# Kernel tuning notes

Hardware: AMD Instinct MI355X
Metric: run time of the kernel (lower is better)

## Reference

```python
import jax, jax.numpy as jnp
import numpy as np

TAU = 0.1  # args.aggregator_tau


def _l2_normalize(x, eps=1e-12):
    # F.normalize(x) : dim=1, p=2, eps clamp on the norm
    n = jnp.linalg.norm(x, axis=1, keepdims=True)
    return x / jnp.maximum(n, eps)


def setup_inputs() -> dict:
    key = jax.random.key(0)
    ks = jax.random.split(key, 9)
    N_LB, N_ULB, D, C = 4096, 6144, 128, 100
    return {
        "anchor_feat": jax.random.normal(ks[0], (N_ULB, D), dtype=jnp.float32),
        "positive_feat": jax.random.normal(ks[1], (N_ULB, D), dtype=jnp.float32),
        "lb_feat": jax.random.normal(ks[2], (N_LB, D), dtype=jnp.float32),
        "lb_one_hot": jax.random.uniform(ks[3], (N_LB, C), dtype=jnp.float32),
        "logits_x_lb": jax.random.normal(ks[4], (N_LB, C), dtype=jnp.float32),
        "logits_x_ulb_1": jax.random.normal(ks[5], (N_ULB, C), dtype=jnp.float32),
        "logits_x_ulb_2": jax.random.normal(ks[6], (N_ULB, C), dtype=jnp.float32),
        "labels_lb": jax.random.randint(ks[7], (N_LB,), 0, C, dtype=jnp.int64),
        "labels_ulb": jax.random.randint(ks[8], (N_ULB,), 0, C, dtype=jnp.int64),
    }


def reference(anchor_feat, positive_feat, lb_feat, lb_one_hot,
              logits_x_lb, logits_x_ulb_1, logits_x_ulb_2,
              labels_lb, labels_ulb):
    normed_lb = _l2_normalize(lb_feat)
    anchor_q = _l2_normalize(anchor_feat)
    positive_q = _l2_normalize(positive_feat)
    # [N, D] with N = N_lb + 2*N_ulb
    feats = jnp.concatenate([normed_lb, anchor_q, positive_q], axis=0)
    logits_before = jnp.concatenate([logits_x_lb, logits_x_ulb_1, logits_x_ulb_2], axis=0)  # [N, C]

    # topk(k=1) over classes
    pred_before = jnp.argmax(logits_before, axis=1)            # [N]
    max_before = jnp.max(logits_before, axis=1)                # [N]

    # non-parametric self-attention aggregation: softmax(FF^T/tau) @ logits
    sim = (feats @ feats.T) / TAU                              # [N, N] large intermediate
    attn = jax.nn.softmax(sim, axis=1)
    logits_after = attn @ logits_before                        # [N, C]

    pred_after = jnp.argmax(logits_after, axis=1)
    max_after = jnp.max(logits_after, axis=1)

    changed = pred_before != pred_after                        # [N] bool
    # Original applies Softmax(dim=1) to [M,1,1] slices of the k=1 top logits,
    # which is identically 1.0, so diff_agg is all zeros; replicate literally.
    diff = jnp.abs(jax.nn.softmax(max_before[:, None], axis=1)
                   - jax.nn.softmax(max_after[:, None], axis=1))[:, 0]  # [N], zeros

    # argmax/argmin restricted to changed indices (first changed idx under ties,
    # matching torch argmax over changed_pred_idx-ordered zeros)
    max_diff_idx = jnp.argmax(jnp.where(changed, diff, -jnp.inf))
    min_diff_idx = jnp.argmin(jnp.where(changed, diff, jnp.inf))

    pred_max_diff_bf = pred_before[max_diff_idx]
    pred_max_diff_af = pred_after[max_diff_idx]
    pred_min_diff_bf = pred_before[min_diff_idx]
    pred_min_diff_af = pred_after[min_diff_idx]

    num_lb = logits_x_lb.shape[0]
    out_lb = logits_after[:num_lb]
    out_ulb = logits_after[num_lb:]
    n_ulb = out_ulb.shape[0] // 2
    out_ulb_1, out_ulb_2 = out_ulb[:n_ulb], out_ulb[n_ulb:]

    return (anchor_feat, positive_feat, lb_feat, lb_one_hot,
            out_lb, out_ulb_1, out_ulb_2,
            max_diff_idx, min_diff_idx,
            pred_max_diff_bf, pred_max_diff_af,
            pred_min_diff_bf, pred_min_diff_af)
```

## Files before the change

### kernel.cpp

```cpp
#include <hip/hip_runtime.h>
#include <hip/hip_bf16.h>

typedef unsigned short u16;
typedef unsigned int u32;
typedef __attribute__((ext_vector_type(8))) short short8;
typedef __attribute__((ext_vector_type(4))) float f32x4;

#define N_LB   4096
#define N_ULB  6144
#define N_TOT  16384
#define D      128
#define C      100
#define CT     104
#define PSTR   104

#define OFF_ANCHOR 0
#define OFF_POS    786432
#define OFF_LBF    1572864
#define OFF_OH     2097152
#define OFF_OUTLB  2506752
#define OFF_SCAL   4145152

__device__ __forceinline__ void split_bf16(float x, u16& hi, u16& lo) {
    __hip_bfloat16 h = __float2bfloat16(x);
    float r = x - __bfloat162float(h);
    __hip_bfloat16 l = __float2bfloat16(r);
    hi = __bfloat16_as_ushort(h);
    lo = __bfloat16_as_ushort(l);
}

__device__ __forceinline__ void gl_lds16(const char* g, char* l) {
    __builtin_amdgcn_global_load_lds(
        (const __attribute__((address_space(1))) u32*)g,
        (__attribute__((address_space(3))) u32*)l, 16, 0, 0);
}

__global__ void prep_all(const float* __restrict__ anchor,
                         const float* __restrict__ positive,
                         const float* __restrict__ lbf,
                         const float* __restrict__ l_lb,
                         const float* __restrict__ l_u1,
                         const float* __restrict__ l_u2,
                         u16* __restrict__ F2, u16* __restrict__ LT,
                         int* __restrict__ predB,
                         float* __restrict__ out)
{
    const int r = blockIdx.x;
    const int t = threadIdx.x;
    const float* fsrc; const float* lsrc; int rr, ptbase;
    if (r < N_LB)              { fsrc = lbf;      lsrc = l_lb; rr = r;                ptbase = OFF_LBF; }
    else if (r < N_LB + N_ULB) { fsrc = anchor;   lsrc = l_u1; rr = r - N_LB;         ptbase = OFF_ANCHOR; }
    else                       { fsrc = positive; lsrc = l_u2; rr = r - N_LB - N_ULB; ptbase = OFF_POS; }

    float2 x = *(const float2*)&fsrc[rr * D + 2 * t];
    float ss = x.x * x.x + x.y * x.y;
    #pragma unroll
    for (int m = 32; m; m >>= 1) ss += __shfl_xor(ss, m);
    float inv = 1.0f / fmaxf(sqrtf(ss), 1e-12f);
    u16 h0, l0, h1, l1;
    split_bf16(x.x * inv, h0, l0);
    split_bf16(x.y * inv, h1, l1);
    *(u32*)&F2[r * 256 + 2 * t]       = (u32)h0 | ((u32)h1 << 16);
    *(u32*)&F2[r * 256 + 128 + 2 * t] = (u32)l0 | ((u32)l1 << 16);
    *(float2*)&out[ptbase + rr * D + 2 * t] = x;

    const int pc = (r & ~31) | (((r >> 2) & 3) << 3) | ((r & 3) << 1) | ((r >> 4) & 1);
    float v0 = lsrc[rr * C + t];
    const int c1 = t + 64;
    float v1 = (c1 < C) ? lsrc[rr * C + c1] : 0.0f;
    u16 h, l;
    split_bf16(v0, h, l);
    LT[(size_t)(0 * CT + t) * N_TOT + pc] = h;
    LT[(size_t)(1 * CT + t) * N_TOT + pc] = l;
    if (c1 < CT) {
        float v = (c1 < C) ? v1 : ((c1 == C) ? 1.0f : 0.0f);
        split_bf16(v, h, l);
        LT[(size_t)(0 * CT + c1) * N_TOT + pc] = h;
        LT[(size_t)(1 * CT + c1) * N_TOT + pc] = l;
    }
    float bv = v0; int bi = t;
    if (c1 < C && v1 > bv) { bv = v1; bi = c1; }
    #pragma unroll
    for (int m = 32; m; m >>= 1) {
        float ov = __shfl_xor(bv, m);
        int   oi = __shfl_xor(bi, m);
        if (ov > bv || (ov == bv && oi < bi)) { bv = ov; bi = oi; }
    }
    if (t == 0) predB[r] = bi;
}

__global__ void copy_oh(const float4* __restrict__ oh, float4* __restrict__ out)
{
    for (int i = blockIdx.x * blockDim.x + threadIdx.x; i < N_LB * C / 4;
         i += gridDim.x * blockDim.x)
        out[i] = oh[i];
}

#define SK_BYTES  (64 * 512)
#define SLT_BYTES (112 * 256)

__launch_bounds__(512, 1)
__global__ void attn_mfma(const u16* __restrict__ F2, const u16* __restrict__ LT,
                          float* __restrict__ parts)
{
    __shared__ __align__(16) char smem[2 * SK_BYTES + 2 * SLT_BYTES];
    char* const sK0  = smem;
    char* const sK1  = smem + SK_BYTES;
    char* const sLT0 = smem + 2 * SK_BYTES;
    char* const sLT1 = smem + 2 * SK_BYTES + SLT_BYTES;

    const int tid  = threadIdx.x;
    const int lane = tid & 63;
    const int w    = tid >> 6;
    const int mq   = w >> 1;
    const int nqh  = w & 1;
    const int g    = lane >> 4;
    const int lr   = lane & 15;
    const int kh   = blockIdx.x & 1;
    const int qb   = blockIdx.x >> 1;
    const int q0   = qb * 128;
    const int KB0  = kh * 8192;

    const char* F2b = (const char*)F2;
    const char* LTb = (const char*)LT;

    if (tid < 256) {
        char* dst = (tid >> 7) ? sLT1 : sLT0;
        int row = 104 + ((tid & 127) >> 4), gr = tid & 15;
        *(f32x4*)(dst + row * 256 + gr * 16) = f32x4{0, 0, 0, 0};
    }

    short8 qhi[2][4], qlo[2][4];
    #pragma unroll
    for (int ms = 0; ms < 2; ++ms) {
        const char* base = F2b + (size_t)(q0 + mq * 32 + ms * 16 + lr) * 512;
        #pragma unroll
        for (int ks = 0; ks < 4; ++ks) {
            qhi[ms][ks] = *(const short8*)(base + ks * 64 + g * 16);
            qlo[ms][ks] = *(const short8*)(base + 256 + ks * 64 + g * 16);
        }
    }

    #pragma unroll
    for (int it = 0; it < 4; ++it) {
        int idx = tid + it * 512;
        int row = idx >> 5, b = (idx & 31) << 4;
        gl_lds16(F2b + (size_t)(KB0 + row) * 512 + (b ^ ((row & 15) << 4)),
                 sK0 + idx * 16);
    }
    #pragma unroll
    for (int it = 0; it < 4; ++it) {
        int idx = tid + it * 512;
        if (idx < 1664) {
            int row = idx >> 4, b = (idx & 15) << 4;
            int b2 = b ^ ((row & 7) << 4);
            int pl = b2 >> 7, kb2 = b2 & 127;
            gl_lds16(LTb + ((size_t)(pl * CT + row) * N_TOT + KB0) * 2 + kb2,
                     sLT0 + idx * 16);
        }
    }

    f32x4 o[2][7];
    #pragma unroll
    for (int ms = 0; ms < 2; ++ms)
        #pragma unroll
        for (int ct = 0; ct < 7; ++ct) o[ms][ct] = f32x4{0, 0, 0, 0};

    for (int ch = 0; ch < 128; ++ch) {
        const int cur = ch & 1;
        __syncthreads();

        if (ch + 1 < 128) {
            const int cn = KB0 + (ch + 1) * 64;
            char* dK = cur ? sK0 : sK1;
            char* dL = cur ? sLT0 : sLT1;
            #pragma unroll
            for (int it = 0; it < 4; ++it) {
                int idx = tid + it * 512;
                int row = idx >> 5, b = (idx & 31) << 4;
                gl_lds16(F2b + (size_t)(cn + row) * 512 + (b ^ ((row & 15) << 4)),
                         dK + idx * 16);
            }
            #pragma unroll
            for (int it = 0; it < 4; ++it) {
                int idx = tid + it * 512;
                if (idx < 1664) {
                    int row = idx >> 4, b = (idx & 15) << 4;
                    int b2 = b ^ ((row & 7) << 4);
                    int pl = b2 >> 7, kb2 = b2 & 127;
                    gl_lds16(LTb + ((size_t)(pl * CT + row) * N_TOT + cn) * 2 + kb2,
                             dL + idx * 16);
                }
            }
        }

        const char* K = cur ? sK1 : sK0;
        u16 h[2][2][4], l[2][2][4];
        #pragma unroll
        for (int t = 0; t < 2; ++t) {
            const int krow = nqh * 32 + t * 16 + lr;
            const int sw = (krow & 15) << 4;
            short8 khi[4], klo[4];
            #pragma unroll
            for (int ks = 0; ks < 4; ++ks) {
                int bo = ks * 64 + g * 16;
                khi[ks] = *(const short8*)(K + krow * 512 + (bo ^ sw));
                klo[ks] = *(const short8*)(K + krow * 512 + ((256 + bo) ^ sw));
            }
            #pragma unroll
            for (int ms = 0; ms < 2; ++ms) {
                f32x4 acc = {0, 0, 0, 0};
                __builtin_amdgcn_s_setprio(1);
                #pragma unroll
                for (int ks = 0; ks < 4; ++ks)
                    acc = __builtin_amdgcn_mfma_f32_16x16x32_bf16(khi[ks], qhi[ms][ks], acc, 0, 0, 0);
                #pragma unroll
                for (int ks = 0; ks < 4; ++ks)
                    acc = __builtin_amdgcn_mfma_f32_16x16x32_bf16(khi[ks], qlo[ms][ks], acc, 0, 0, 0);
                #pragma unroll
                for (int ks = 0; ks < 4; ++ks)
                    acc = __builtin_amdgcn_mfma_f32_16x16x32_bf16(klo[ks], qhi[ms][ks], acc, 0, 0, 0);
                __builtin_amdgcn_s_setprio(0);
                #pragma unroll
                for (int reg = 0; reg < 4; ++reg) {
                    float p = __expf(10.0f * acc[reg] - 10.0f);
                    split_bf16(p, h[ms][t][reg], l[ms][t][reg]);
                }
            }
        }

        const char* Lt = cur ? sLT1 : sLT0;
        short8 Ahi[2], Alo[2];
        #pragma unroll
        for (int ms = 0; ms < 2; ++ms) {
            Ahi[ms] = short8{(short)h[ms][0][0], (short)h[ms][1][0],
                             (short)h[ms][0][1], (short)h[ms][1][1],
                             (short)h[ms][0][2], (short)h[ms][1][2],
                             (short)h[ms][0][3], (short)h[ms][1][3]};
            Alo[ms] = short8{(short)l[ms][0][0], (short)l[ms][1][0],
                             (short)l[ms][0][1], (short)l[ms][1][1],
                             (short)l[ms][0][2], (short)l[ms][1][2],
                             (short)l[ms][0][3], (short)l[ms][1][3]};
        }
        __builtin_amdgcn_s_setprio(1);
        #pragma unroll
        for (int ct = 0; ct < 7; ++ct) {
            int cls = ct * 16 + lr;
            int swc = (cls & 7) << 4;
            int boh = (nqh * 64 + g * 16) ^ swc;
            int bol = 128 + boh;
            short8 Bhi = *(const short8*)(Lt + cls * 256 + boh);
            short8 Blo = *(const short8*)(Lt + cls * 256 + bol);
            #pragma unroll
            for (int ms = 0; ms < 2; ++ms) {
                o[ms][ct] = __builtin_amdgcn_mfma_f32_16x16x32_bf16(Ahi[ms], Bhi, o[ms][ct], 0, 0, 0);
                o[ms][ct] = __builtin_amdgcn_mfma_f32_16x16x32_bf16(Ahi[ms], Blo, o[ms][ct], 0, 0, 0);
                o[ms][ct] = __builtin_amdgcn_mfma_f32_16x16x32_bf16(Alo[ms], Bhi, o[ms][ct], 0, 0, 0);
            }
        }
        __builtin_amdgcn_s_setprio(0);
    }

    __syncthreads();
    float* red = (float*)smem;
    if (nqh == 1) {
        #pragma unroll
        for (int ms = 0; ms < 2; ++ms)
            #pragma unroll
            for (int ct = 0; ct < 7; ++ct)
                #pragma unroll
                for (int reg = 0; reg < 4; ++reg)
                    red[(((mq * 2 + ms) * 7) + ct) * 256 + reg * 64 + lane] = o[ms][ct][reg];
    }
    __syncthreads();
    if (nqh == 0) {
        #pragma unroll
        for (int ms = 0; ms < 2; ++ms) {
            #pragma unroll
            for (int ct = 0; ct < 7; ++ct) {
                int cls = ct * 16 + lr;
                if (cls < PSTR) {
                    #pragma unroll
                    for (int reg = 0; reg < 4; ++reg) {
                        int q = q0 + mq * 32 + ms * 16 + g * 4 + reg;
                        float v = o[ms][ct][reg] +
                                  red[(((mq * 2 + ms) * 7) + ct) * 256 + reg * 64 + lane];
                        parts[(size_t)(kh * N_TOT + q) * PSTR + cls] = v;
                    }
                }
            }
        }
    }
}

__global__ void reduce_argmax(const float* __restrict__ parts,
                              float* __restrict__ out, int* __restrict__ predA)
{
    const int lane = threadIdx.x & 63;
    const int row  = blockIdx.x * 4 + (threadIdx.x >> 6);
    const float* p0 = parts + (size_t)row * PSTR;
    const float* p1 = parts + (size_t)(N_TOT + row) * PSTR;
    const float inv = 1.0f / (p0[100] + p1[100]);
    float v0 = (p0[lane] + p1[lane]) * inv;
    out[OFF_OUTLB + (size_t)row * C + lane] = v0;
    float bv = v0; int bi = lane;
    const int c1 = lane + 64;
    if (c1 < C) {
        float v1 = (p0[c1] + p1[c1]) * inv;
        out[OFF_OUTLB + (size_t)row * C + c1] = v1;
        if (v1 > bv) { bv = v1; bi = c1; }
    }
    #pragma unroll
    for (int m = 32; m; m >>= 1) {
        float ov = __shfl_xor(bv, m);
        int   oi = __shfl_xor(bi, m);
        if (ov > bv || (ov == bv && oi < bi)) { bv = ov; bi = oi; }
    }
    if (lane == 0) predA[row] = bi;
}

__global__ void finalize(const int* __restrict__ predA, const int* __restrict__ predB,
                         float* __restrict__ out)
{
    __shared__ int sm[256];
    const int t = threadIdx.x;
    int local = N_TOT;
    for (int r = t; r < N_TOT; r += 256)
        if (predA[r] != predB[r] && r < local) local = r;
    sm[t] = local;
    __syncthreads();
    for (int s = 128; s; s >>= 1) {
        if (t < s) sm[t] = min(sm[t], sm[t + s]);
        __syncthreads();
    }
    if (t == 0) {
        int first = (sm[0] == N_TOT) ? 0 : sm[0];
        out[OFF_SCAL + 0] = (float)first;
        out[OFF_SCAL + 1] = (float)first;
        out[OFF_SCAL + 2] = (float)predB[first];
        out[OFF_SCAL + 3] = (float)predA[first];
        out[OFF_SCAL + 4] = (float)predB[first];
        out[OFF_SCAL + 5] = (float)predA[first];
    }
}

extern "C" void kernel_launch(void* const* d_in, const int* in_sizes, int n_in,
                              void* d_out, int out_size, void* d_ws, size_t ws_size,
                              hipStream_t stream)
{
    const float* anchor   = (const float*)d_in[0];
    const float* positive = (const float*)d_in[1];
    const float* lbf      = (const float*)d_in[2];
    const float* oh       = (const float*)d_in[3];
    const float* l_lb     = (const float*)d_in[4];
    const float* l_u1     = (const float*)d_in[5];
    const float* l_u2     = (const float*)d_in[6];
    float* out = (float*)d_out;

    u16* F2 = (u16*)d_ws;
    u16* LT = F2 + (size_t)N_TOT * 256;
    float* parts = (float*)(LT + (size_t)2 * CT * N_TOT);
    int* predB = (int*)(parts + (size_t)2 * N_TOT * PSTR);
    int* predA = predB + N_TOT;

    prep_all  <<<N_TOT, 64, 0, stream>>>(anchor, positive, lbf, l_lb, l_u1, l_u2,
                                         F2, LT, predB, out);
    copy_oh   <<<200, 256, 0, stream>>>((const float4*)oh, (float4*)&out[OFF_OH]);
    attn_mfma <<<256, 512, 0, stream>>>(F2, LT, parts);
    reduce_argmax<<<N_TOT / 4, 256, 0, stream>>>(parts, out, predA);
    finalize  <<<1, 256, 0, stream>>>(predA, predB, out);
}
```

Measured before the change: 343.3 us.

## Software-pipeline attention loop: overlap exp of chunk with PV MFMAs of previous

Restructures the main loop so the P@V MFMAs for the previous chunk run right after the QK^T MFMAs of the current chunk, while the exp and bf16 split of the current scores is deferred. This lets VALU exp work interleave with matrix work from another stage. The LT buffer moves from double to triple buffering to hold the extra in-flight chunk, which costs more LDS. Global addresses are now advanced incrementally instead of recomputed each iteration, the exp uses exp2f with an FMA, and the setprio hints are removed.

After: 361.2 us. 5.2% more time.

```diff
diff --git a/kernel.cpp b/kernel.cpp
--- a/kernel.cpp
+++ b/kernel.cpp
@@ -20,6 +20,8 @@
 #define OFF_OH     2097152
 #define OFF_OUTLB  2506752
 #define OFF_SCAL   4145152
+
+#define LOG2E10 14.4269504088896f
 
 __device__ __forceinline__ void split_bf16(float x, u16& hi, u16& lo) {
     __hip_bfloat16 h = __float2bfloat16(x);
@@ -103,11 +105,12 @@
 __global__ void attn_mfma(const u16* __restrict__ F2, const u16* __restrict__ LT,
                           float* __restrict__ parts)
 {
-    __shared__ __align__(16) char smem[2 * SK_BYTES + 2 * SLT_BYTES];
+    __shared__ __align__(16) char smem[2 * SK_BYTES + 3 * SLT_BYTES];
     char* const sK0  = smem;
     char* const sK1  = smem + SK_BYTES;
     char* const sLT0 = smem + 2 * SK_BYTES;
     char* const sLT1 = smem + 2 * SK_BYTES + SLT_BYTES;
+    char* const sLT2 = smem + 2 * SK_BYTES + 2 * SLT_BYTES;
 
     const int tid  = threadIdx.x;
     const int lane = tid & 63;
@@ -124,8 +127,9 @@
     const char* F2b = (const char*)F2;
     const char* LTb = (const char*)LT;
 
-    if (tid < 256) {
-        char* dst = (tid >> 7) ? sLT1 : sLT0;
+    if (tid < 384) {
+        int bf = tid >> 7;
+        char* dst = (bf == 0) ? sLT0 : (bf == 1) ? sLT1 : sLT2;
         int row = 104 + ((tid & 127) >> 4), gr = tid & 15;
         *(f32x4*)(dst + row * 256 + gr * 16) = f32x4{0, 0, 0, 0};
     }
@@ -141,24 +145,33 @@
         }
     }
 
+    const char* gK[4]; const char* gL[4]; int dKo[4], dLo[4]; bool lOK[4];
     #pragma unroll
     for (int it = 0; it < 4; ++it) {
         int idx = tid + it * 512;
         int row = idx >> 5, b = (idx & 31) << 4;
-        gl_lds16(F2b + (size_t)(KB0 + row) * 512 + (b ^ ((row & 15) << 4)),
-                 sK0 + idx * 16);
+        gK[it] = F2b + (size_t)(KB0 + row) * 512 + (b ^ ((row & 15) << 4));
+        dKo[it] = idx * 16;
     }
     #pragma unroll
     for (int it = 0; it < 4; ++it) {
         int idx = tid + it * 512;
-        if (idx < 1664) {
-            int row = idx >> 4, b = (idx & 15) << 4;
-            int b2 = b ^ ((row & 7) << 4);
-            int pl = b2 >> 7, kb2 = b2 & 127;
-            gl_lds16(LTb + ((size_t)(pl * CT + row) * N_TOT + KB0) * 2 + kb2,
-                     sLT0 + idx * 16);
-        }
-    }
+        lOK[it] = (idx < 1664);
+        int row = idx >> 4, b = (idx & 15) << 4;
+        int b2 = b ^ ((row & 7) << 4);
+        int pl = b2 >> 7, kb2 = b2 & 127;
+        gL[it] = LTb + ((size_t)(pl * CT + row) * N_TOT + KB0) * 2 + kb2;
+        dLo[it] = idx * 16;
+    }
+
+    char* Lprev = sLT2;
+    char* Lcur  = sLT0;
+    char* Lnext = sLT1;
+
+    #pragma unroll
+    for (int it = 0; it < 4; ++it) gl_lds16(gK[it], sK0 + dKo[it]);
+    #pragma unroll
+    for (int it = 0; it < 4; ++it) if (lOK[it]) gl_lds16(gL[it], Lcur + dLo[it]);
 
     f32x4 o[2][7];
     #pragma unroll
@@ -166,36 +179,28 @@
         #pragma unroll
         for (int ct = 0; ct < 7; ++ct) o[ms][ct] = f32x4{0, 0, 0, 0};
 
+    short8 Ahi_p[2], Alo_p[2];
+
     for (int ch = 0; ch < 128; ++ch) {
-        const int cur = ch & 1;
         __syncthreads();
 
+        char* Kc = (ch & 1) ? sK1 : sK0;
+        char* Kn = (ch & 1) ? sK0 : sK1;
+
         if (ch + 1 < 128) {
-            const int cn = KB0 + (ch + 1) * 64;
-            char* dK = cur ? sK0 : sK1;
-            char* dL = cur ? sLT0 : sLT1;
             #pragma unroll
             for (int it = 0; it < 4; ++it) {
-                int idx = tid + it * 512;
-                int row = idx >> 5, b = (idx & 31) << 4;
-                gl_lds16(F2b + (size_t)(cn + row) * 512 + (b ^ ((row & 15) << 4)),
-                         dK + idx * 16);
+                gK[it] += 64 * 512;
+                gl_lds16(gK[it], Kn + dKo[it]);
             }
             #pragma unroll
             for (int it = 0; it < 4; ++it) {
-                int idx = tid + it * 512;
-                if (idx < 1664) {
-                    int row = idx >> 4, b = (idx & 15) << 4;
-                    int b2 = b ^ ((row & 7) << 4);
-                    int pl = b2 >> 7, kb2 = b2 & 127;
-                    gl_lds16(LTb + ((size_t)(pl * CT + row) * N_TOT + cn) * 2 + kb2,
-                             dL + idx * 16);
-                }
-            }
-        }
-
-        const char* K = cur ? sK1 : sK0;
-        u16 h[2][2][4], l[2][2][4];
+                gL[it] += 64 * 2;
+                if (lOK[it]) gl_lds16(gL[it], Lnext + dLo[it]);
+            }
+        }
+
+        f32x4 sacc[2][2];
         #pragma unroll
         for (int t = 0; t < 2; ++t) {
             const int krow = nqh * 32 + t * 16 + lr;
@@ -204,13 +209,12 @@
             #pragma unroll
             for (int ks = 0; ks < 4; ++ks) {
                 int bo = ks * 64 + g * 16;
-                khi[ks] = *(const short8*)(K + krow * 512 + (bo ^ sw));
-                klo[ks] = *(const short8*)(K + krow * 512 + ((256 + bo) ^ sw));
+                khi[ks] = *(const short8*)(Kc + krow * 512 + (bo ^ sw));
+                klo[ks] = *(const short8*)(Kc + krow * 512 + ((256 + bo) ^ sw));
             }
             #pragma unroll
             for (int ms = 0; ms < 2; ++ms) {
                 f32x4 acc = {0, 0, 0, 0};
-                __builtin_amdgcn_s_setprio(1);
                 #pragma unroll
                 for (int ks = 0; ks < 4; ++ks)
                     acc = __builtin_amdgcn_mfma_f32_16x16x32_bf16(khi[ks], qhi[ms][ks], acc, 0, 0, 0);
@@ -220,45 +224,69 @@
                 #pragma unroll
                 for (int ks = 0; ks < 4; ++ks)
                     acc = __builtin_amdgcn_mfma_f32_16x16x32_bf16(klo[ks], qhi[ms][ks], acc, 0, 0, 0);
-                __builtin_amdgcn_s_setprio(0);
-                #pragma unroll
-                for (int reg = 0; reg < 4; ++reg) {
-                    float p = __expf(10.0f * acc[reg] - 10.0f);
-                    split_bf16(p, h[ms][t][reg], l[ms][t][reg]);
+                sacc[ms][t] = acc;
+            }
+        }
+
+        if (ch) {
+            #pragma unroll
+            for (int ct = 0; ct < 7; ++ct) {
+                int cls = ct * 16 + lr;
+                int swc = (cls & 7) << 4;
+                int boh = (nqh * 64 + g * 16) ^ swc;
+                int bol = 128 + boh;
+                short8 Bhi = *(const short8*)(Lprev + cls * 256 + boh);
+                short8 Blo = *(const short8*)(Lprev + cls * 256 + bol);
+                #pragma unroll
+                for (int ms = 0; ms < 2; ++ms) {
+                    o[ms][ct] = __builtin_amdgcn_mfma_f32_16x16x32_bf16(Ahi_p[ms], Bhi, o[ms][ct], 0, 0, 0);
+                    o[ms][ct] = __builtin_amdgcn_mfma_f32_16x16x32_bf16(Ahi_p[ms], Blo, o[ms][ct], 0, 0, 0);
+                    o[ms][ct] = __builtin_amdgcn_mfma_f32_16x16x32_bf16(Alo_p[ms], Bhi, o[ms][ct], 0, 0, 0);
                 }
             }
         }
 
-        const char* Lt = cur ? sLT1 : sLT0;
-        short8 Ahi[2], Alo[2];
+        {
+            u16 h[2][2][4], l[2][2][4];
+            #pragma unroll
+            for (int ms = 0; ms < 2; ++ms)
+                #pragma unroll
+                for (int t = 0; t < 2; ++t)
+                    #pragma unroll
+                    for (int reg = 0; reg < 4; ++reg) {
+                        float p = exp2f(fmaf(LOG2E10, sacc[ms][t][reg], -LOG2E10));
+                        split_bf16(p, h[ms][t][reg], l[ms][t][reg]);
+                    }
+            #pragma unroll
+            for (int ms = 0; ms < 2; ++ms) {
+                Ahi_p[ms] = short8{(short)h[ms][0][0], (short)h[ms][1][0],
+                                   (short)h[ms][0][1], (short)h[ms][1][1],
+                                   (short)h[ms][0][2], (short)h[ms][1][2],
+                                   (short)h[ms][0][3], (short)h[ms][1][3]};
+                Alo_p[ms] = short8{(short)l[ms][0][0], (short)l[ms][1][0],
+                                   (short)l[ms][0][1], (short)l[ms][1][1],
+                                   (short)l[ms][0][2], (short)l[ms][1][2],
+                                   (short)l[ms][0][3], (short)l[ms][1][3]};
+            }
+        }
+
+        char* tmp = Lprev; Lprev = Lcur; Lcur = Lnext; Lnext = tmp;
+    }
+
+    #pragma unroll
+    for (int ct = 0; ct < 7; ++ct) {
+        int cls = ct * 16 + lr;
+        int swc = (cls & 7) << 4;
+        int boh = (nqh * 64 + g * 16) ^ swc;
+        int bol = 128 + boh;
+        short8 Bhi = *(const short8*)(Lprev + cls * 256 + boh);
+        short8 Blo = *(const short8*)(Lprev + cls * 256 + bol);
         #pragma unroll
         for (int ms = 0; ms < 2; ++ms) {
-            Ahi[ms] = short8{(short)h[ms][0][0], (short)h[ms][1][0],
-                             (short)h[ms][0][1], (short)h[ms][1][1],
-                             (short)h[ms][0][2], (short)h[ms][1][2],
-                             (short)h[ms][0][3], (short)h[ms][1][3]};
-            Alo[ms] = short8{(short)l[ms][0][0], (short)l[ms][1][0],
-                             (short)l[ms][0][1], (short)l[ms][1][1],
-                             (short)l[ms][0][2], (short)l[ms][1][2],
-                             (short)l[ms][0][3], (short)l[ms][1][3]};
-        }
-        __builtin_amdgcn_s_setprio(1);
-        #pragma unroll
-        for (int ct = 0; ct < 7; ++ct) {
-            int cls = ct * 16 + lr;
-            int swc = (cls & 7) << 4;
-            int boh = (nqh * 64 + g * 16) ^ swc;
-            int bol = 128 + boh;
-            short8 Bhi = *(const short8*)(Lt + cls * 256 + boh);
-            short8 Blo = *(const short8*)(Lt + cls * 256 + bol);
-            #pragma unroll
-            for (int ms = 0; ms < 2; ++ms) {
-                o[ms][ct] = __builtin_amdgcn_mfma_f32_16x16x32_bf16(Ahi[ms], Bhi, o[ms][ct], 0, 0, 0);
-                o[ms][ct] = __builtin_amdgcn_mfma_f32_16x16x32_bf16(Ahi[ms], Blo, o[ms][ct], 0, 0, 0);
-                o[ms][ct] = __builtin_amdgcn_mfma_f32_16x16x32_bf16(Alo[ms], Bhi, o[ms][ct], 0, 0, 0);
-            }
-        }
-        __builtin_amdgcn_s_setprio(0);
+            o[ms][ct] = __builtin_amdgcn_mfma_f32_16x16x32_bf16(Ahi_p[ms], Bhi, o[ms][ct], 0, 0, 0);
+            o[ms][ct] = __builtin_amdgcn_mfma_f32_16x16x32_bf16(Ahi_p[ms], Blo, o[ms][ct], 0, 0, 0);
+            o[ms][ct] = __builtin_amdgcn_mfma_f32_16x16x32_bf16(Alo_p[ms], Bhi, o[ms][ct], 0, 0, 0);
+        }
     }
 
     __syncthreads();
```
